# Optimization experiments

Measured on AMD Instinct MI355X. Metric: run time of the kernel, lower is better.

## Reference

```python
import jax, jax.numpy as jnp
import numpy as np

B, T, N = 512, 1024, 64


def setup_inputs() -> dict:
    key = jax.random.key(0)
    k1, k2, k3 = jax.random.split(key, 3)
    unary = jax.random.normal(k1, (B, T, N), dtype=jnp.float32)
    lengths = jax.random.randint(k2, (B,), 1, T + 1)
    transitions = jax.random.normal(k3, (N, N), dtype=jnp.float32) * 0.1
    return {"unary": unary, "lengths": lengths, "transitions": transitions}


def reference(unary, lengths, transitions):
    # CRF log-partition (forward algorithm), same math as tf.contrib.crf.crf_log_norm.
    # unary: [B, T, N], lengths: [B], transitions: [N, N] -> logZ: [B]
    Bs, Ts, Ns = unary.shape
    lengths = jnp.maximum(lengths, 1)
    alpha0 = unary[:, 0, :]  # [B, N]

    # scan over time steps 1..T-1; freeze alpha once t >= length (dynamic_rnn semantics)
    unary_rest = jnp.swapaxes(unary[:, 1:, :], 0, 1)  # [T-1, B, N]
    ts = jnp.arange(1, Ts)

    def step(alpha, inp):
        u_t, t = inp
        # scores[b, i, j] = alpha[b, i] + transitions[i, j] + u_t[b, j]
        scores = alpha[:, :, None] + transitions[None, :, :] + u_t[:, None, :]
        new_alpha = jax.nn.logsumexp(scores, axis=1)  # [B, N]
        alpha = jnp.where((t < lengths)[:, None], new_alpha, alpha)
        return alpha, None

    alpha, _ = jax.lax.scan(step, alpha0, (unary_rest, ts))
    return jax.nn.logsumexp(alpha, axis=1)  # [B]
```

## Files before the change

### kernel.cpp

```cpp
#include <hip/hip_runtime.h>


typedef float f2 __attribute__((ext_vector_type(2)));
typedef float f4 __attribute__((ext_vector_type(4)));

constexpr int Tt = 1024;
constexpr int Nn = 64;
constexpr int ES  = 68;
constexpr int EPS = 68;
constexpr float LN2 = 0.69314718055994530942f;

__device__ __forceinline__ float xsum32(float x) {
    float a = x, b = x;
    asm("s_nop 1\n\tv_permlane32_swap_b32 %0, %1" : "+v"(a), "+v"(b));
    return a + b;
}

__global__ __launch_bounds__(128, 1) void crf_fwd(
    const float* __restrict__ unary,
    const int*   __restrict__ lengths,
    const float* __restrict__ trans,
    float*       __restrict__ out)
{
    const int b    = blockIdx.x;
    const int tid  = threadIdx.x;
    const int w    = tid >> 6;
    const int lane = tid & 63;
    const int q    = lane & 31;
    const int h    = lane >> 5;

    __shared__ float Erow[Nn * ES];
    __shared__ float Eperm[128 * EPS];
    __shared__ __align__(16) float shp[2][Nn];
    __shared__ float shb[Nn];
    __shared__ int   sh_off_b;

    #pragma unroll
    for (int c = 0; c < (Nn * Nn) / 128; ++c) {
        int idx = c * 128 + tid;
        Erow[(idx >> 6) * ES + (idx & 63)] = __expf(trans[idx]);
    }
    __syncthreads();

    float* ep = &Eperm[tid * EPS];
    #pragma unroll
    for (int v = 0; v < 64; ++v) {
        int o = q + 32 * (v >> 5);
        int i = 32 * h + (v & 31);
        ep[v] = (w == 0) ? Erow[i * ES + o] : Erow[o * ES + i];
    }

    const f4* eb = (const f4*)ep;
    f4 EA0  = eb[0],  EA1  = eb[1],  EA2  = eb[2],  EA3  = eb[3];
    f4 EA4  = eb[4],  EA5  = eb[5],  EA6  = eb[6],  EA7  = eb[7];
    f4 EA8  = eb[8],  EA9  = eb[9],  EA10 = eb[10], EA11 = eb[11];
    f4 EA12 = eb[12], EA13 = eb[13], EA14 = eb[14], EA15 = eb[15];
    asm volatile("" : "+v"(EA0),  "+v"(EA1),  "+v"(EA2),  "+v"(EA3),
                      "+v"(EA4),  "+v"(EA5),  "+v"(EA6),  "+v"(EA7),
                      "+v"(EA8),  "+v"(EA9),  "+v"(EA10), "+v"(EA11),
                      "+v"(EA12), "+v"(EA13), "+v"(EA14), "+v"(EA15));

    int L = lengths[b];
    L = L < 1 ? 1 : (L > Tt ? Tt : L);
    const int m2 = (L - 1) >> 1;

    const float* ub = unary + (size_t)b * Tt * Nn;

    const int trips = (w == 0) ? m2 : (L - 1 - m2);
    const int tbase = (w == 0) ? 1 : (L - 1);
    const int dir   = (w == 0) ? 1 : -1;

    float acc = (w == 0) ? __expf(ub[lane]) : 1.0f;
    int   off = 0;

    float* myp = shp[w];
    const f4* rowp = (const f4*)&shp[w][32 * h];

    const int smax = trips > 0 ? trips - 1 : 0;
    float wq0, wq1, wq2, wq3, uq0, uq1, uq2, uq3;
    {
        int c0 = 0 < smax ? 0 : smax, c1 = 1 < smax ? 1 : smax;
        int c2 = 2 < smax ? 2 : smax, c3 = 3 < smax ? 3 : smax;
        wq0 = __expf(ub[(tbase + dir * c0) * Nn + lane]);
        wq1 = __expf(ub[(tbase + dir * c1) * Nn + lane]);
        wq2 = __expf(ub[(tbase + dir * c2) * Nn + lane]);
        wq3 = __expf(ub[(tbase + dir * c3) * Nn + lane]);
        int c4 = 4 < smax ? 4 : smax, c5 = 5 < smax ? 5 : smax;
        int c6 = 6 < smax ? 6 : smax, c7 = 7 < smax ? 7 : smax;
        uq0 = ub[(tbase + dir * c4) * Nn + lane];
        uq1 = ub[(tbase + dir * c5) * Nn + lane];
        uq2 = ub[(tbase + dir * c6) * Nn + lane];
        uq3 = ub[(tbase + dir * c7) * Nn + lane];
    }

    for (int s0 = 0; s0 < trips; s0 += 4) {
        float un0, un1, un2, un3, wn0, wn1, wn2, wn3;
        {
            int c0 = s0 + 8,  c1 = s0 + 9,  c2 = s0 + 10, c3 = s0 + 11;
            c0 = c0 > smax ? smax : c0;  c1 = c1 > smax ? smax : c1;
            c2 = c2 > smax ? smax : c2;  c3 = c3 > smax ? smax : c3;
            un0 = ub[(tbase + dir * c0) * Nn + lane];
            un1 = ub[(tbase + dir * c1) * Nn + lane];
            un2 = ub[(tbase + dir * c2) * Nn + lane];
            un3 = ub[(tbase + dir * c3) * Nn + lane];
        }
        wn0 = __expf(uq0); wn1 = __expf(uq1);
        wn2 = __expf(uq2); wn3 = __expf(uq3);

        #pragma unroll
        for (int k = 0; k < 4; ++k) {
            if (s0 + k >= trips) break;

            float wk = (k == 0) ? wq0 : (k == 1) ? wq1 : (k == 2) ? wq2 : wq3;

            float src = (w != 0) ? acc * wk : acc;

            myp[lane] = src;
            f4 av0 = rowp[0], av1 = rowp[1], av2 = rowp[2], av3 = rowp[3];
            f4 av4 = rowp[4], av5 = rowp[5], av6 = rowp[6], av7 = rowp[7];

            f4 Aa = av0 * EA0;       f4 Ab = av1 * EA1;
            Aa = av2 * EA2 + Aa;     Ab = av3 * EA3 + Ab;
            Aa = av4 * EA4 + Aa;     Ab = av5 * EA5 + Ab;
            Aa = av6 * EA6 + Aa;     Ab = av7 * EA7 + Ab;
            f4 Ba = av0 * EA8;       f4 Bb = av1 * EA9;
            Ba = av2 * EA10 + Ba;    Bb = av3 * EA11 + Bb;
            Ba = av4 * EA12 + Ba;    Bb = av5 * EA13 + Bb;
            Ba = av6 * EA14 + Ba;    Bb = av7 * EA15 + Bb;

            f4 At = Aa + Ab;         f4 Bt = Ba + Bb;
            f2 Ah = At.xy + At.zw;   f2 Bh = Bt.xy + Bt.zw;
            float Pa = Ah[0] + Ah[1];
            float Pb = Bh[0] + Bh[1];

            float za = xsum32(Pa);
            float zb = xsum32(Pb);
            float z  = (lane & 32) ? zb : za;

            acc = (w == 0) ? z * wk : z;
        }

        {
            unsigned s0b = (unsigned)__builtin_amdgcn_readfirstlane(
                (int)__float_as_uint(acc));
            int e = (int)((s0b >> 23) & 0xFF) - 127;
            off += e;
            acc *= __uint_as_float((unsigned)(127 - e) << 23);
        }

        wq0 = wn0; wq1 = wn1; wq2 = wn2; wq3 = wn3;
        uq0 = un0; uq1 = un1; uq2 = un2; uq3 = un3;
    }

    if (w == 1) {
        shb[lane] = acc;
        if (lane == 0) sh_off_b = off;
    }
    __syncthreads();
    if (w == 0) {
        float v = acc * shb[lane];
        float ssum = v;
        #pragma unroll
        for (int k = 32; k >= 1; k >>= 1)
            ssum += __shfl_xor(ssum, k, 64);
        if (lane == 0) {
            float l2 = __builtin_amdgcn_logf(ssum);
            out[b] = LN2 * ((float)(off + sh_off_b) + l2);
        }
    }
}

extern "C" void kernel_launch(void* const* d_in, const int* in_sizes, int n_in,
                              void* d_out, int out_size, void* d_ws, size_t ws_size,
                              hipStream_t stream) {
    const float* unary   = (const float*)d_in[0];
    const int*   lengths = (const int*)d_in[1];
    const float* trans   = (const float*)d_in[2];
    float*       out     = (float*)d_out;

    const int Bb = in_sizes[1];
    crf_fwd<<<Bb, 128, 0, stream>>>(unary, lengths, trans, out);
}
```

Baseline: 295.4 us.

## Sort chains by length and pair short with long chains per block

Adds a ranking kernel that sorts batch indices by sequence length, then launches half as many 256-thread blocks, each processing two chains (the k-th shortest and k-th longest) with two waves each. This balances per-block work so the tail is not dominated by the longest chains, and halves block count relative to 256 CUs. It also drops the Eperm shared staging buffer, loading transition values straight from Erow into registers. It adds an extra O(B^2) ranking launch, and for odd B the middle chain is computed twice by both halves of one block.

```diff
diff --git a/kernel.cpp b/kernel.cpp
--- a/kernel.cpp
+++ b/kernel.cpp
@@ -6,8 +6,7 @@
 
 constexpr int Tt = 1024;
 constexpr int Nn = 64;
-constexpr int ES  = 68;
-constexpr int EPS = 68;
+constexpr int ES = 68;
 constexpr float LN2 = 0.69314718055994530942f;
 
 __device__ __forceinline__ float xsum32(float x) {
@@ -16,65 +15,91 @@
     return a + b;
 }
 
-__global__ __launch_bounds__(128, 1) void crf_fwd(
+__global__ __launch_bounds__(512) void rank_pairs(
+    const int* __restrict__ lengths, int* __restrict__ perm, int Bb)
+{
+    for (int i = threadIdx.x; i < Bb; i += 512) {
+        int Li = lengths[i];
+        int rank = 0;
+        for (int j = 0; j < Bb; ++j) {
+            int Lj = lengths[j];
+            rank += (Lj < Li) || (Lj == Li && j < i);
+        }
+        perm[rank] = i;
+    }
+}
+
+__global__ __launch_bounds__(256, 1) void crf_fwd(
     const float* __restrict__ unary,
     const int*   __restrict__ lengths,
     const float* __restrict__ trans,
-    float*       __restrict__ out)
+    const int*   __restrict__ perm,
+    float*       __restrict__ out,
+    int Bb)
 {
-    const int b    = blockIdx.x;
     const int tid  = threadIdx.x;
-    const int w    = tid >> 6;
+    const int w4   = tid >> 6;
+    const int dirW = w4 & 1;
+    const int c    = w4 >> 1;
     const int lane = tid & 63;
     const int q    = lane & 31;
     const int h    = lane >> 5;
 
     __shared__ float Erow[Nn * ES];
-    __shared__ float Eperm[128 * EPS];
-    __shared__ __align__(16) float shp[2][Nn];
-    __shared__ float shb[Nn];
-    __shared__ int   sh_off_b;
+    __shared__ __align__(16) float shp[4][Nn];
+    __shared__ float shb[2][Nn];
+    __shared__ int   sh_off_b[2];
 
     #pragma unroll
-    for (int c = 0; c < (Nn * Nn) / 128; ++c) {
-        int idx = c * 128 + tid;
+    for (int ci = 0; ci < (Nn * Nn) / 256; ++ci) {
+        int idx = ci * 256 + tid;
         Erow[(idx >> 6) * ES + (idx & 63)] = __expf(trans[idx]);
     }
     __syncthreads();
 
-    float* ep = &Eperm[tid * EPS];
-    #pragma unroll
-    for (int v = 0; v < 64; ++v) {
+    const int chain = perm[(c == 0) ? blockIdx.x : (Bb - 1 - blockIdx.x)];
+
+    auto EL = [&](int v) -> float {
         int o = q + 32 * (v >> 5);
         int i = 32 * h + (v & 31);
-        ep[v] = (w == 0) ? Erow[i * ES + o] : Erow[o * ES + i];
-    }
-
-    const f4* eb = (const f4*)ep;
-    f4 EA0  = eb[0],  EA1  = eb[1],  EA2  = eb[2],  EA3  = eb[3];
-    f4 EA4  = eb[4],  EA5  = eb[5],  EA6  = eb[6],  EA7  = eb[7];
-    f4 EA8  = eb[8],  EA9  = eb[9],  EA10 = eb[10], EA11 = eb[11];
-    f4 EA12 = eb[12], EA13 = eb[13], EA14 = eb[14], EA15 = eb[15];
+        return (dirW == 0) ? Erow[i * ES + o] : Erow[o * ES + i];
+    };
+    f4 EA0  = {EL(0),  EL(1),  EL(2),  EL(3)};
+    f4 EA1  = {EL(4),  EL(5),  EL(6),  EL(7)};
+    f4 EA2  = {EL(8),  EL(9),  EL(10), EL(11)};
+    f4 EA3  = {EL(12), EL(13), EL(14), EL(15)};
+    f4 EA4  = {EL(16), EL(17), EL(18), EL(19)};
+    f4 EA5  = {EL(20), EL(21), EL(22), EL(23)};
+    f4 EA6  = {EL(24), EL(25), EL(26), EL(27)};
+    f4 EA7  = {EL(28), EL(29), EL(30), EL(31)};
+    f4 EA8  = {EL(32), EL(33), EL(34), EL(35)};
+    f4 EA9  = {EL(36), EL(37), EL(38), EL(39)};
+    f4 EA10 = {EL(40), EL(41), EL(42), EL(43)};
+    f4 EA11 = {EL(44), EL(45), EL(46), EL(47)};
+    f4 EA12 = {EL(48), EL(49), EL(50), EL(51)};
+    f4 EA13 = {EL(52), EL(53), EL(54), EL(55)};
+    f4 EA14 = {EL(56), EL(57), EL(58), EL(59)};
+    f4 EA15 = {EL(60), EL(61), EL(62), EL(63)};
     asm volatile("" : "+v"(EA0),  "+v"(EA1),  "+v"(EA2),  "+v"(EA3),
                       "+v"(EA4),  "+v"(EA5),  "+v"(EA6),  "+v"(EA7),
                       "+v"(EA8),  "+v"(EA9),  "+v"(EA10), "+v"(EA11),
                       "+v"(EA12), "+v"(EA13), "+v"(EA14), "+v"(EA15));
 
-    int L = lengths[b];
+    int L = lengths[chain];
     L = L < 1 ? 1 : (L > Tt ? Tt : L);
     const int m2 = (L - 1) >> 1;
 
-    const float* ub = unary + (size_t)b * Tt * Nn;
-
-    const int trips = (w == 0) ? m2 : (L - 1 - m2);
-    const int tbase = (w == 0) ? 1 : (L - 1);
-    const int dir   = (w == 0) ? 1 : -1;
-
-    float acc = (w == 0) ? __expf(ub[lane]) : 1.0f;
+    const float* ub = unary + (size_t)chain * Tt * Nn;
+
+    const int trips = (dirW == 0) ? m2 : (L - 1 - m2);
+    const int tbase = (dirW == 0) ? 1 : (L - 1);
+    const int dir   = (dirW == 0) ? 1 : -1;
+
+    float acc = (dirW == 0) ? __expf(ub[lane]) : 1.0f;
     int   off = 0;
 
-    float* myp = shp[w];
-    const f4* rowp = (const f4*)&shp[w][32 * h];
+    float* myp = shp[w4];
+    const f4* rowp = (const f4*)&shp[w4][32 * h];
 
     const int smax = trips > 0 ? trips - 1 : 0;
     float wq0, wq1, wq2, wq3, uq0, uq1, uq2, uq3;
@@ -113,7 +138,7 @@
 
             float wk = (k == 0) ? wq0 : (k == 1) ? wq1 : (k == 2) ? wq2 : wq3;
 
-            float src = (w != 0) ? acc * wk : acc;
+            float src = (dirW != 0) ? acc * wk : acc;
 
             myp[lane] = src;
             f4 av0 = rowp[0], av1 = rowp[1], av2 = rowp[2], av3 = rowp[3];
@@ -137,7 +162,7 @@
             float zb = xsum32(Pb);
             float z  = (lane & 32) ? zb : za;
 
-            acc = (w == 0) ? z * wk : z;
+            acc = (dirW == 0) ? z * wk : z;
         }
 
         {
@@ -152,20 +177,20 @@
         uq0 = un0; uq1 = un1; uq2 = un2; uq3 = un3;
     }
 
-    if (w == 1) {
-        shb[lane] = acc;
-        if (lane == 0) sh_off_b = off;
+    if (dirW == 1) {
+        shb[c][lane] = acc;
+        if (lane == 0) sh_off_b[c] = off;
     }
     __syncthreads();
-    if (w == 0) {
-        float v = acc * shb[lane];
+    if (dirW == 0) {
+        float v = acc * shb[c][lane];
         float ssum = v;
         #pragma unroll
         for (int k = 32; k >= 1; k >>= 1)
             ssum += __shfl_xor(ssum, k, 64);
         if (lane == 0) {
             float l2 = __builtin_amdgcn_logf(ssum);
-            out[b] = LN2 * ((float)(off + sh_off_b) + l2);
+            out[chain] = LN2 * ((float)(off + sh_off_b[c]) + l2);
         }
     }
 }
@@ -177,7 +202,10 @@
     const int*   lengths = (const int*)d_in[1];
     const float* trans   = (const float*)d_in[2];
     float*       out     = (float*)d_out;
+    int*         perm    = (int*)d_ws;
 
     const int Bb = in_sizes[1];
-    crf_fwd<<<Bb, 128, 0, stream>>>(unary, lengths, trans, out);
-}
+    rank_pairs<<<1, 512, 0, stream>>>(lengths, perm, Bb);
+    crf_fwd<<<(Bb + 1) / 2, 256, 0, stream>>>(unary, lengths, trans, perm,
+                                              out, Bb);
+}
```

Measured after the change: 287.9 us. 2.5% less time.
